# Optimization experiments

Hardware: AMD Instinct MI355X
Metric: run time of the kernel (lower is better)

The kernel has to match this reference:

```python
import jax, jax.numpy as jnp
import numpy as np

N_FEAT = 64
N_PROJ = 32
N_OUT = 128
LN_EPS = 1e-5


def setup_inputs() -> dict:
    key = jax.random.key(0)
    ks = jax.random.split(key, 8)
    n_seq, n_res = 256, 384
    M = jax.random.normal(ks[0], (1, n_seq, n_res, N_FEAT), dtype=jnp.float32)
    M_mask = jnp.ones((1, n_seq, n_res), dtype=jnp.float32)
    Z_raw = jax.random.normal(ks[1], (1, n_res, n_res, N_OUT), dtype=jnp.float32)
    s = 1.0 / np.sqrt(N_FEAT)
    Wa = jax.random.uniform(ks[2], (N_PROJ, N_FEAT), jnp.float32, -s, s)
    ba = jnp.zeros((N_PROJ,), jnp.float32)
    Wb = jax.random.uniform(ks[3], (N_PROJ, N_FEAT), jnp.float32, -s, s)
    bb = jnp.zeros((N_PROJ,), jnp.float32)
    so = 1.0 / np.sqrt(N_PROJ * N_PROJ)
    Wo = jax.random.uniform(ks[4], (N_OUT, N_PROJ * N_PROJ), jnp.float32, -so, so)
    bo = jnp.zeros((N_OUT,), jnp.float32)
    gamma = jnp.ones((N_FEAT,), jnp.float32)
    beta = jnp.zeros((N_FEAT,), jnp.float32)
    return {"M": M, "M_mask": M_mask, "Z_raw": Z_raw, "gamma": gamma, "beta": beta,
            "Wa": Wa, "ba": ba, "Wb": Wb, "bb": bb, "Wo": Wo, "bo": bo}


def reference(M, M_mask, Z_raw, gamma, beta, Wa, ba, Wb, bb, Wo, bo):
    # LayerNorm over last dim
    mu = jnp.mean(M, axis=-1, keepdims=True)
    var = jnp.mean(jnp.square(M - mu), axis=-1, keepdims=True)
    Mn = (M - mu) * jax.lax.rsqrt(var + LN_EPS) * gamma + beta
    # projections [1, s, r, p]
    left = jnp.einsum('bsrf,pf->bsrp', Mn, Wa) + ba
    right = jnp.einsum('bsrf,pf->bsrp', Mn, Wb) + bb
    mask = M_mask[..., None]  # [1, s, r, 1]
    left = mask * left
    right = mask * right
    # norm[i,j] = sum_s mask[s,i]*mask[s,j]
    norm = jnp.einsum('sa,sd->ad', M_mask[0], M_mask[0])[None, :, :, None]
    n_res, p = left.shape[2], left.shape[3]
    # outer-product mean: O[i,j,c,d] = sum_s left[s,i,c] * right[s,j,d]
    O = jnp.einsum('sic,sjd->ijcd', left[0], right[0])
    O = O.reshape(n_res, n_res, p * p)
    Z = jnp.einsum('ijk,ok->ijo', O, Wo) + bo  # [r, r, n_out]
    Z = Z[None] / (0.001 + norm)
    return Z + Z_raw
```

## Files before the change

### kernel.cpp

```cpp
#include <hip/hip_runtime.h>

typedef unsigned short u16;
typedef u16   u16x4 __attribute__((ext_vector_type(4)));
typedef u16   u16x8 __attribute__((ext_vector_type(8)));
typedef short s16x8 __attribute__((ext_vector_type(8)));
typedef float f32x4 __attribute__((ext_vector_type(4)));

#define NSEQ 256
#define NRES 384
#define NF   64
#define NP   32
#define NO   128

__device__ __forceinline__ u16 f2b(float f) {
    union { float f; unsigned u; } c; c.f = f;
    unsigned r = c.u + 0x7fffu + ((c.u >> 16) & 1u);
    return (u16)(r >> 16);
}
__device__ __forceinline__ float b2f(u16 h) {
    union { unsigned u; float f; } c; c.u = ((unsigned)h) << 16;
    return c.f;
}

__device__ __forceinline__ void gload_lds16(const u16* g, u16* l) {
    __builtin_amdgcn_global_load_lds(
        (const __attribute__((address_space(1))) unsigned int*)(g),
        (__attribute__((address_space(3))) unsigned int*)(l),
        16, 0, 0);
}

__global__ __launch_bounds__(256) void k_pre(
    const float* __restrict__ M, const float* __restrict__ mask,
    const float* __restrict__ gamma, const float* __restrict__ beta,
    const float* __restrict__ Wa, const float* __restrict__ ba,
    const float* __restrict__ Wb, const float* __restrict__ bb,
    const float* __restrict__ Wo,
    u16* __restrict__ leftT, u16* __restrict__ rightT,
    float* __restrict__ normMat, u16* __restrict__ WoB)
{
    __shared__ __align__(16) char sm[52480];
    const int b = blockIdx.x, t = threadIdx.x;

    if (b < 768) {
        const int sC = b / 24, iC = b % 24;
        const int i0 = iC * 16, s0 = sC * 8;

        u16*   hiP   = (u16*)sm;
        u16*   loP   = (u16*)sm + 8192;
        u16*   WP    = (u16*)(sm + 32768);
        float* mkP   = (float*)(sm + 51200);
        float* biasP = (float*)(sm + 51712);
        float* glP   = (float*)(sm + 51968);
        float* blP   = (float*)(sm + 52224);

        const int wv = t >> 6, ln = t & 63;
        const int quad = ln >> 4, l16 = ln & 15;

        {
            const int rl = ln >> 4, c = ln & 15;
            #pragma unroll
            for (int q = 0; q < 8; ++q) {
                int rbase = wv * 32 + q * 4;
                int r   = rbase + rl;
                int xsw = (r & 3) << 1;
                const float* src = M + ((long)(s0 + (r & 7)) * NRES + (i0 + (r >> 3))) * NF
                                     + ((c ^ xsw) << 2);
                gload_lds16((const u16*)src, (u16*)sm + rbase * 128);
            }
        }
        {
            const int side = t >> 7, p = (t >> 2) & 31, qq = t & 3;
            const float* Wg = (side ? Wb : Wa) + p * 64 + qq * 16;
            u16x8 h[2], l[2];
            #pragma unroll
            for (int u = 0; u < 4; ++u) {
                f32x4 w4 = *(const f32x4*)(Wg + u * 4);
                #pragma unroll
                for (int e = 0; e < 4; ++e) {
                    u16 hb = f2b(w4[e]);
                    h[u >> 1][(u & 1) * 4 + e] = hb;
                    l[u >> 1][(u & 1) * 4 + e] = f2b(w4[e] - b2f(hb));
                }
            }
            int hbase = ((side * 2 + 0) * 32 + p) * 72 + qq * 16;
            int lbase = ((side * 2 + 1) * 32 + p) * 72 + qq * 16;
            *(u16x8*)(WP + hbase)     = h[0];
            *(u16x8*)(WP + hbase + 8) = h[1];
            *(u16x8*)(WP + lbase)     = l[0];
            *(u16x8*)(WP + lbase + 8) = l[1];
        }
        if (t < 128) mkP[t] = mask[(long)(s0 + (t & 7)) * NRES + i0 + (t >> 3)];
        if (t < 64) { glP[t] = gamma[t]; blP[t] = beta[t];
                      biasP[t] = (t < 32) ? ba[t] : bb[t - 32]; }
        __syncthreads();

        const int r = t >> 1, half = t & 1;
        const int xsw = (r & 3) << 1, psw = r & 3;
        f32x4 v[8];
        {
            const float* raw = (const float*)sm + r * 64;
            #pragma unroll
            for (int e = 0; e < 8; ++e)
                v[e] = *(const f32x4*)(raw + (((half * 8 + e) ^ xsw) << 2));
        }
        float sum = 0.f, sq = 0.f;
        #pragma unroll
        for (int e = 0; e < 8; ++e)
            #pragma unroll
            for (int j = 0; j < 4; ++j) { float x = v[e][j]; sum += x; sq += x * x; }
        sum += __shfl_xor(sum, 1); sq += __shfl_xor(sq, 1);
        float mu  = sum * (1.f / 64.f);
        float var = sq * (1.f / 64.f) - mu * mu;
        float rs  = rsqrtf(var + 1e-5f);
        #pragma unroll
        for (int e = 0; e < 8; ++e) {
            int og = half * 8 + e;
            f32x4 g4 = *(const f32x4*)(glP + og * 4);
            f32x4 b4 = *(const f32x4*)(blP + og * 4);
            #pragma unroll
            for (int j = 0; j < 4; ++j) v[e][j] = (v[e][j] - mu) * rs * g4[j] + b4[j];
        }
        __syncthreads();

        #pragma unroll
        for (int d = 0; d < 4; ++d) {
            u16x8 h8, l8;
            #pragma unroll
            for (int j = 0; j < 4; ++j) {
                u16 hb = f2b(v[2 * d][j]);
                h8[j] = hb; l8[j] = f2b(v[2 * d][j] - b2f(hb));
                u16 hb2 = f2b(v[2 * d + 1][j]);
                h8[4 + j] = hb2; l8[4 + j] = f2b(v[2 * d + 1][j] - b2f(hb2));
            }
            int q = (half * 4 + d) ^ psw;
            *(u16x8*)(hiP + r * 64 + q * 8) = h8;
            *(u16x8*)(loP + r * 64 + q * 8) = l8;
        }
        __syncthreads();

        const int wbase = wv * 32;
        f32x4 acc[2][4] = {};
        #pragma unroll
        for (int k = 0; k < 2; ++k) {
            u16x8 ah[2], al[2];
            #pragma unroll
            for (int rt = 0; rt < 2; ++rt) {
                int row = wbase + rt * 16 + l16;
                int gk  = (quad + k * 4) ^ (row & 3);
                ah[rt] = *(const u16x8*)(hiP + row * 64 + gk * 8);
                al[rt] = *(const u16x8*)(loP + row * 64 + gk * 8);
            }
            #pragma unroll
            for (int pt = 0; pt < 4; ++pt) {
                int side = pt >> 1, ph = pt & 1;
                int hrow = ((side * 2 + 0) * 32 + ph * 16 + l16) * 72 + (quad + k * 4) * 8;
                int lrow = ((side * 2 + 1) * 32 + ph * 16 + l16) * 72 + (quad + k * 4) * 8;
                u16x8 bh = *(const u16x8*)(WP + hrow);
                u16x8 bl = *(const u16x8*)(WP + lrow);
                #pragma unroll
                for (int rt = 0; rt < 2; ++rt) {
                    acc[rt][pt] = __builtin_amdgcn_mfma_f32_16x16x32_bf16(
                        (s16x8)ah[rt], (s16x8)bh, acc[rt][pt], 0, 0, 0);
                    acc[rt][pt] = __builtin_amdgcn_mfma_f32_16x16x32_bf16(
                        (s16x8)al[rt], (s16x8)bh, acc[rt][pt], 0, 0, 0);
                    acc[rt][pt] = __builtin_amdgcn_mfma_f32_16x16x32_bf16(
                        (s16x8)ah[rt], (s16x8)bl, acc[rt][pt], 0, 0, 0);
                }
            }
        }

        #pragma unroll
        for (int rt = 0; rt < 2; ++rt) {
            int rowb = wbase + rt * 16 + quad * 4;
            f32x4 mk4 = *(const f32x4*)(mkP + rowb);
            int ii = rowb >> 3, sb = rowb & 7;
            #pragma unroll
            for (int pt = 0; pt < 4; ++pt) {
                int side = pt >> 1, p = (pt & 1) * 16 + l16;
                float bv = biasP[side * 32 + p];
                u16x4 ov;
                #pragma unroll
                for (int rg = 0; rg < 4; ++rg)
                    ov[rg] = f2b((acc[rt][pt][rg] + bv) * mk4[rg]);
                u16* dst = (side ? rightT : leftT)
                         + ((long)(i0 + ii) * NP + p) * NSEQ + s0 + sb;
                *(u16x4*)dst = ov;
            }
        }

    } else if (b < 896) {
        int idx = (b - 768) * 256 + t;
        int o   = idx >> 8;
        int kp  = (idx & 255) << 2;
        int l16 = (kp >> 2) & 15;
        int ntb = (kp >> 6) & 1;
        int qd  = (kp >> 7) & 3;
        int mtb = (kp >> 9) & 1;
        const float* src = Wo + o * 1024 + (mtb * 16 + qd * 4) * 32 + ntb * 16 + l16;
        u16x4 w;
        #pragma unroll
        for (int rg = 0; rg < 4; ++rg) w[rg] = f2b(src[rg * 32]);
        *(u16x4*)(WoB + o * 1024 + kp) = w;

    } else {
        float (*mi)[17] = (float (*)[17])sm;
        float (*mj)[17] = (float (*)[17])(sm + 17408);
        const int bn = b - 896;
        const int iB = (bn / 24) * 16, jB = (bn % 24) * 16;
        #pragma unroll
        for (int it = 0; it < 16; ++it) {
            int ss = it * 16 + (t >> 4);
            int c  = t & 15;
            mi[ss][c] = mask[(long)ss * NRES + iB + c];
            mj[ss][c] = mask[(long)ss * NRES + jB + c];
        }
        __syncthreads();
        const int ti = t >> 4, tj = t & 15;
        float acc = 0.f;
        for (int ss = 0; ss < 256; ++ss) acc += mi[ss][ti] * mj[ss][tj];
        normMat[(long)(iB + ti) * NRES + jB + tj] = acc;
    }
}

__global__ __launch_bounds__(512, 4) void k_main(
    const u16* __restrict__ leftT, const u16* __restrict__ rightT,
    const float* __restrict__ normMat,
    const u16* __restrict__ WoB, const float* __restrict__ bo,
    const float* __restrict__ Zraw, float* __restrict__ out)
{
    __shared__ __align__(16) u16 smem[32768];

    const int t    = threadIdx.x;
    const int wave = t >> 6, lane = t & 63;
    const int quad = lane >> 4, l16 = lane & 15;
    const int wr = wave >> 1, wc = wave & 1;

    const int bid = blockIdx.x;
    const int r_  = bid >> 3;
    const int bx  = r_ / 12;
    const int by  = (bid & 7) * 12 + (r_ % 12);
    const int icBase = bx * 256;
    const int jdBase = by * 128;

    const int srow = lane >> 2;
    const int g8   = ((lane & 3) ^ ((srow >> 1) & 3)) * 8;

    f32x4 acc[4][4] = {};

    const u16* aSrc0 = leftT  + (icBase + wave * 32 + srow) * NSEQ + g8;
    const u16* aSrc1 = aSrc0 + 16 * NSEQ;
    const u16* bSrc  = rightT + (jdBase + wave * 16 + srow) * NSEQ + g8;

    #define STAGE(buf, k0) do {                                                  \
        gload_lds16(aSrc0 + (k0), &smem[(buf) * 8192 + wave * 1024]);            \
        gload_lds16(aSrc1 + (k0), &smem[(buf) * 8192 + wave * 1024 + 512]);      \
        gload_lds16(bSrc  + (k0), &smem[16384 + (buf) * 4096 + wave * 512]);     \
    } while (0)

    STAGE(0, 0);

    #pragma unroll
    for (int kt = 0; kt < 8; ++kt) {
        const int cur = kt & 1;
        if (kt < 7) {
            STAGE(cur ^ 1, (kt + 1) * 32);
            asm volatile("s_waitcnt vmcnt(3)" ::: "memory");
        } else {
            asm volatile("s_waitcnt vmcnt(0)" ::: "memory");
        }
        __builtin_amdgcn_s_barrier();
        __builtin_amdgcn_sched_barrier(0);

        const int gx = (quad ^ ((l16 >> 1) & 3)) * 8;
        u16x8 af[4], bf[4];
        const u16* Ab = &smem[cur * 8192 + (wr * 64 + l16) * 32 + gx];
        const u16* Bb = &smem[16384 + cur * 4096 + (wc * 64 + l16) * 32 + gx];
        #pragma unroll
        for (int mt = 0; mt < 4; ++mt) af[mt] = *(const u16x8*)(Ab + mt * 512);
        #pragma unroll
        for (int nt = 0; nt < 4; ++nt) bf[nt] = *(const u16x8*)(Bb + nt * 512);

        __builtin_amdgcn_s_setprio(1);
        #pragma unroll
        for (int mt = 0; mt < 4; ++mt)
            #pragma unroll
            for (int nt = 0; nt < 4; ++nt)
                acc[mt][nt] = __builtin_amdgcn_mfma_f32_16x16x32_bf16(
                    (s16x8)af[mt], (s16x8)bf[nt], acc[mt][nt], 0, 0, 0);
        __builtin_amdgcn_s_setprio(0);

        __builtin_amdgcn_sched_barrier(0);
        __builtin_amdgcn_s_barrier();
    }
    #undef STAGE

    #pragma unroll
    for (int mt = 0; mt < 4; ++mt) {
        #pragma unroll
        for (int nt = 0; nt < 4; ++nt) {
            int pair = (wr * 2 + (mt >> 1)) * 4 + wc * 2 + (nt >> 1);
            int kp   = l16 * 4 + (nt & 1) * 64 + quad * 128 + (mt & 1) * 512;
            int ks   = kp ^ (quad << 4) ^ ((pair & 7) << 3);
            u16x4 wv;
            #pragma unroll
            for (int rg = 0; rg < 4; ++rg) wv[rg] = f2b(acc[mt][nt][rg]);
            *(u16x4*)&smem[pair * 1024 + ks] = wv;
        }
    }
    __syncthreads();

    f32x4 acc2[2] = {};
    const int ob   = wave * 16;
    const int pxor = (l16 & 7) << 3;
    const u16* wp  = WoB + (ob + l16) * 1024 + quad * 8;
    const u16* os0 = &smem[l16 * 1024];
    const u16* os1 = &smem[(16 + l16) * 1024];
    #pragma unroll 8
    for (int kk = 0; kk < 32; ++kk) {
        int kp = kk * 32 + quad * 8;
        int ks = kp ^ (((kp >> 7) & 3) << 4) ^ pxor;
        u16x8 a0 = *(const u16x8*)(os0 + ks);
        u16x8 a1 = *(const u16x8*)(os1 + ks);
        u16x8 bv = *(const u16x8*)(wp + kk * 32);
        __builtin_amdgcn_s_setprio(1);
        acc2[0] = __builtin_amdgcn_mfma_f32_16x16x32_bf16((s16x8)a0, (s16x8)bv, acc2[0], 0, 0, 0);
        acc2[1] = __builtin_amdgcn_mfma_f32_16x16x32_bf16((s16x8)a1, (s16x8)bv, acc2[1], 0, 0, 0);
        __builtin_amdgcn_s_setprio(0);
    }
    __syncthreads();

    float* zs = (float*)smem;
    #pragma unroll
    for (int m = 0; m < 2; ++m)
        #pragma unroll
        for (int rg = 0; rg < 4; ++rg)
            zs[(m * 16 + quad * 4 + rg) * 128 + ob + l16] = acc2[m][rg];
    __syncthreads();

    const int i0 = bx * 8, j0 = by * 4;
    const int pr = t >> 4, o0 = (t & 15) * 8;
    const int i = i0 + (pr >> 2), j = j0 + (pr & 3);
    const float rn = 1.f / (0.001f + normMat[i * NRES + j]);
    const long base = ((long)(i * NRES + j)) * NO + o0;
    f32x4 z0  = *(const f32x4*)&zs[pr * 128 + o0];
    f32x4 z1  = *(const f32x4*)&zs[pr * 128 + o0 + 4];
    f32x4 zr0 = *(const f32x4*)(Zraw + base);
    f32x4 zr1 = *(const f32x4*)(Zraw + base + 4);
    f32x4 bv0 = *(const f32x4*)(bo + o0);
    f32x4 bv1 = *(const f32x4*)(bo + o0 + 4);
    f32x4 r0, r1;
    #pragma unroll
    for (int e = 0; e < 4; ++e) r0[e] = (z0[e] + bv0[e]) * rn + zr0[e];
    #pragma unroll
    for (int e = 0; e < 4; ++e) r1[e] = (z1[e] + bv1[e]) * rn + zr1[e];
    *(f32x4*)(out + base)     = r0;
    *(f32x4*)(out + base + 4) = r1;
}

extern "C" void kernel_launch(void* const* d_in, const int* in_sizes, int n_in,
                              void* d_out, int out_size, void* d_ws, size_t ws_size,
                              hipStream_t stream)
{
    const float* M     = (const float*)d_in[0];
    const float* mask  = (const float*)d_in[1];
    const float* Zraw  = (const float*)d_in[2];
    const float* gamma = (const float*)d_in[3];
    const float* beta  = (const float*)d_in[4];
    const float* Wa    = (const float*)d_in[5];
    const float* ba    = (const float*)d_in[6];
    const float* Wb    = (const float*)d_in[7];
    const float* bb    = (const float*)d_in[8];
    const float* Wo    = (const float*)d_in[9];
    const float* bo    = (const float*)d_in[10];
    float* out = (float*)d_out;

    char* ws = (char*)d_ws;
    u16*   leftT   = (u16*)ws;
    u16*   rightT  = (u16*)(ws + 6291456);
    float* normMat = (float*)(ws + 12582912);
    u16*   WoB     = (u16*)(ws + 13172736);

    k_pre<<<dim3(1472), dim3(256), 0, stream>>>(M, mask, gamma, beta,
                                                Wa, ba, Wb, bb, Wo,
                                                leftT, rightT, normMat, WoB);
    k_main<<<dim3(4608), dim3(512), 0, stream>>>(leftT, rightT, normMat,
                                                 WoB, bo, Zraw, out);
}
```

Before: 341.8 us.

## Triple-buffer outer-product K loop and split Wo GEMM over K halves

The main GEMM loop moves from double to triple buffering, so the next-next stage is issued after a single barrier per iteration instead of two. The second GEMM (outer products times Wo) now gives each wave a 32x32 output tile over half of K. The two K halves are then summed through a padded LDS buffer. This raises MFMA reuse per Wo load and removes one barrier per iteration, at the cost of more LDS (72KB), which may lower occupancy, and two extra reduction syncs.

```diff
diff --git a/kernel.cpp b/kernel.cpp
--- a/kernel.cpp
+++ b/kernel.cpp
@@ -228,7 +228,7 @@
     const u16* __restrict__ WoB, const float* __restrict__ bo,
     const float* __restrict__ Zraw, float* __restrict__ out)
 {
-    __shared__ __align__(16) u16 smem[32768];
+    __shared__ __align__(16) u16 smem[36864];
 
     const int t    = threadIdx.x;
     const int wave = t >> 6, lane = t & 63;
@@ -251,30 +251,28 @@
     const u16* aSrc1 = aSrc0 + 16 * NSEQ;
     const u16* bSrc  = rightT + (jdBase + wave * 16 + srow) * NSEQ + g8;
 
-    #define STAGE(buf, k0) do {                                                  \
-        gload_lds16(aSrc0 + (k0), &smem[(buf) * 8192 + wave * 1024]);            \
-        gload_lds16(aSrc1 + (k0), &smem[(buf) * 8192 + wave * 1024 + 512]);      \
-        gload_lds16(bSrc  + (k0), &smem[16384 + (buf) * 4096 + wave * 512]);     \
+    #define STAGE(bb, k0) do {                                                   \
+        gload_lds16(aSrc0 + (k0), &smem[(bb) * 12288 + wave * 1024]);            \
+        gload_lds16(aSrc1 + (k0), &smem[(bb) * 12288 + wave * 1024 + 512]);      \
+        gload_lds16(bSrc  + (k0), &smem[(bb) * 12288 + 8192 + wave * 512]);      \
     } while (0)
 
     STAGE(0, 0);
+    STAGE(1, 32);
 
     #pragma unroll
     for (int kt = 0; kt < 8; ++kt) {
-        const int cur = kt & 1;
-        if (kt < 7) {
-            STAGE(cur ^ 1, (kt + 1) * 32);
-            asm volatile("s_waitcnt vmcnt(3)" ::: "memory");
-        } else {
-            asm volatile("s_waitcnt vmcnt(0)" ::: "memory");
-        }
+        if (kt < 7) asm volatile("s_waitcnt vmcnt(3)" ::: "memory");
+        else        asm volatile("s_waitcnt vmcnt(0)" ::: "memory");
         __builtin_amdgcn_s_barrier();
         __builtin_amdgcn_sched_barrier(0);
-
+        if (kt < 6) STAGE((kt + 2) % 3, (kt + 2) * 32);
+
+        const int bb = kt % 3;
         const int gx = (quad ^ ((l16 >> 1) & 3)) * 8;
         u16x8 af[4], bf[4];
-        const u16* Ab = &smem[cur * 8192 + (wr * 64 + l16) * 32 + gx];
-        const u16* Bb = &smem[16384 + cur * 4096 + (wc * 64 + l16) * 32 + gx];
+        const u16* Ab = &smem[bb * 12288 + (wr * 64 + l16) * 32 + gx];
+        const u16* Bb = &smem[bb * 12288 + 8192 + (wc * 64 + l16) * 32 + gx];
         #pragma unroll
         for (int mt = 0; mt < 4; ++mt) af[mt] = *(const u16x8*)(Ab + mt * 512);
         #pragma unroll
@@ -288,11 +286,9 @@
                 acc[mt][nt] = __builtin_amdgcn_mfma_f32_16x16x32_bf16(
                     (s16x8)af[mt], (s16x8)bf[nt], acc[mt][nt], 0, 0, 0);
         __builtin_amdgcn_s_setprio(0);
-
-        __builtin_amdgcn_sched_barrier(0);
-        __builtin_amdgcn_s_barrier();
     }
     #undef STAGE
+    __syncthreads();
 
     #pragma unroll
     for (int mt = 0; mt < 4; ++mt) {
@@ -309,32 +305,53 @@
     }
     __syncthreads();
 
-    f32x4 acc2[2] = {};
-    const int ob   = wave * 16;
+    f32x4 acc2[2][2] = {};
+    const int oh = wave & 3, kh = wave >> 2;
+    const int ob = oh * 32;
     const int pxor = (l16 & 7) << 3;
-    const u16* wp  = WoB + (ob + l16) * 1024 + quad * 8;
+    const u16* wp0 = WoB + (long)(ob + l16) * 1024 + kh * 512 + quad * 8;
+    const u16* wp1 = wp0 + 16 * 1024;
     const u16* os0 = &smem[l16 * 1024];
     const u16* os1 = &smem[(16 + l16) * 1024];
     #pragma unroll 8
-    for (int kk = 0; kk < 32; ++kk) {
-        int kp = kk * 32 + quad * 8;
+    for (int kk = 0; kk < 16; ++kk) {
+        int kp = kh * 512 + kk * 32 + quad * 8;
         int ks = kp ^ (((kp >> 7) & 3) << 4) ^ pxor;
         u16x8 a0 = *(const u16x8*)(os0 + ks);
         u16x8 a1 = *(const u16x8*)(os1 + ks);
-        u16x8 bv = *(const u16x8*)(wp + kk * 32);
+        u16x8 b0 = *(const u16x8*)(wp0 + kk * 32);
+        u16x8 b1 = *(const u16x8*)(wp1 + kk * 32);
         __builtin_amdgcn_s_setprio(1);
-        acc2[0] = __builtin_amdgcn_mfma_f32_16x16x32_bf16((s16x8)a0, (s16x8)bv, acc2[0], 0, 0, 0);
-        acc2[1] = __builtin_amdgcn_mfma_f32_16x16x32_bf16((s16x8)a1, (s16x8)bv, acc2[1], 0, 0, 0);
+        acc2[0][0] = __builtin_amdgcn_mfma_f32_16x16x32_bf16((s16x8)a0, (s16x8)b0, acc2[0][0], 0, 0, 0);
+        acc2[0][1] = __builtin_amdgcn_mfma_f32_16x16x32_bf16((s16x8)a0, (s16x8)b1, acc2[0][1], 0, 0, 0);
+        acc2[1][0] = __builtin_amdgcn_mfma_f32_16x16x32_bf16((s16x8)a1, (s16x8)b0, acc2[1][0], 0, 0, 0);
+        acc2[1][1] = __builtin_amdgcn_mfma_f32_16x16x32_bf16((s16x8)a1, (s16x8)b1, acc2[1][1], 0, 0, 0);
         __builtin_amdgcn_s_setprio(0);
     }
     __syncthreads();
 
     float* zs = (float*)smem;
-    #pragma unroll
-    for (int m = 0; m < 2; ++m)
-        #pragma unroll
-        for (int rg = 0; rg < 4; ++rg)
-            zs[(m * 16 + quad * 4 + rg) * 128 + ob + l16] = acc2[m][rg];
+    if (kh == 0) {
+        #pragma unroll
+        for (int ph = 0; ph < 2; ++ph)
+            #pragma unroll
+            for (int n2 = 0; n2 < 2; ++n2)
+                #pragma unroll
+                for (int rg = 0; rg < 4; ++rg)
+                    zs[(ph * 16 + quad * 4 + rg) * 132 + ob + n2 * 16 + l16]
+                        = acc2[ph][n2][rg];
+    }
+    __syncthreads();
+    if (kh == 1) {
+        #pragma unroll
+        for (int ph = 0; ph < 2; ++ph)
+            #pragma unroll
+            for (int n2 = 0; n2 < 2; ++n2)
+                #pragma unroll
+                for (int rg = 0; rg < 4; ++rg)
+                    zs[(ph * 16 + quad * 4 + rg) * 132 + ob + n2 * 16 + l16]
+                        += acc2[ph][n2][rg];
+    }
     __syncthreads();
 
     const int i0 = bx * 8, j0 = by * 4;
@@ -342,8 +359,8 @@
     const int i = i0 + (pr >> 2), j = j0 + (pr & 3);
     const float rn = 1.f / (0.001f + normMat[i * NRES + j]);
     const long base = ((long)(i * NRES + j)) * NO + o0;
-    f32x4 z0  = *(const f32x4*)&zs[pr * 128 + o0];
-    f32x4 z1  = *(const f32x4*)&zs[pr * 128 + o0 + 4];
+    f32x4 z0  = *(const f32x4*)&zs[pr * 132 + o0];
+    f32x4 z1  = *(const f32x4*)&zs[pr * 132 + o0 + 4];
     f32x4 zr0 = *(const f32x4*)(Zraw + base);
     f32x4 zr1 = *(const f32x4*)(Zraw + base + 4);
     f32x4 bv0 = *(const f32x4*)(bo + o0);
```

After: 342.9 us. About the same (+0.3%).
